# Optimization experiments

Hardware: AMD Instinct MI355X
Metric: run time of the kernel (lower is better)

The kernel has to match this reference:

```python
import jax, jax.numpy as jnp
import numpy as np

# --- architecture constants (match init_kwargs) ---
SLEN = 104
PTILE = 8
STEP = 2
N_BANDS = 2
MAX_DET = 2
N_SRC_PARAMS = 2
ENC_C = 20
ENC_HIDDEN = 256
# dim_out_all = 0.5*D*(D+1)*(4+2*n_source_params) + 1 + D  (probs over n_sources + per-count loc/flux mean+logvar)
DIM_OUT = int(0.5 * MAX_DET * (MAX_DET + 1) * (4 + 2 * N_SRC_PARAMS)) + 1 + MAX_DET  # 27


def _p(key, shape, scale=0.02):
    return scale * jax.random.normal(key, shape, dtype=jnp.float32)


def setup_inputs() -> dict:
    key = jax.random.key(0)
    ks = jax.random.split(key, 14)
    flat_in = ENC_C * PTILE * PTILE  # 20*8*8 = 1280
    return {
        "images": jax.random.normal(ks[0], (32, N_BANDS, SLEN, SLEN), dtype=jnp.float32),
        "conv1_w": _p(ks[1], (ENC_C, N_BANDS, 3, 3)),
        "conv1_b": _p(ks[2], (ENC_C,)),
        "conv2_w": _p(ks[3], (ENC_C, ENC_C, 3, 3)),
        "conv2_b": _p(ks[4], (ENC_C,)),
        "fc1_w": _p(ks[5], (ENC_HIDDEN, flat_in)),
        "fc1_b": _p(ks[6], (ENC_HIDDEN,)),
        "fc2_w": _p(ks[7], (ENC_HIDDEN, ENC_HIDDEN)),
        "fc2_b": _p(ks[8], (ENC_HIDDEN,)),
        "fc3_w": _p(ks[9], (ENC_HIDDEN, ENC_HIDDEN)),
        "fc3_b": _p(ks[10], (ENC_HIDDEN,)),
        "fcf_w": _p(ks[11], (DIM_OUT, ENC_HIDDEN)),
        "fcf_b": _p(ks[12], (DIM_OUT,)),
    }


def _tile_images(images):
    # torch tile_images: (B, C, slen, slen) -> (B * n_ptiles, C, P, P), tiles row-major over (x, y)
    B, C = images.shape[0], images.shape[1]
    patches = jax.lax.conv_general_dilated_patches(
        images, filter_shape=(PTILE, PTILE), window_strides=(STEP, STEP), padding="VALID"
    )  # (B, C*P*P, Hn, Wn) with feature dim ordered (C, P, P)
    Hn, Wn = patches.shape[2], patches.shape[3]
    p = patches.reshape(B, C, PTILE, PTILE, Hn, Wn)
    p = p.transpose(0, 4, 5, 1, 2, 3)  # (B, Hn, Wn, C, P, P)
    return p.reshape(B * Hn * Wn, C, PTILE, PTILE)


def _conv(x, w, b):
    y = jax.lax.conv_general_dilated(
        x, w, window_strides=(1, 1), padding="SAME",
        dimension_numbers=("NCHW", "OIHW", "NCHW"),
    )
    return y + b[None, :, None, None]


def reference(images, conv1_w, conv1_b, conv2_w, conv2_b,
              fc1_w, fc1_b, fc2_w, fc2_b, fc3_w, fc3_b, fcf_w, fcf_b):
    ptiles = _tile_images(images)                       # (B*nT, C, P, P)
    h = jax.nn.relu(_conv(ptiles, conv1_w, conv1_b))    # (B*nT, 20, P, P)
    h = jax.nn.relu(_conv(h, conv2_w, conv2_b))
    h = h.reshape(h.shape[0], -1)                       # Flatten -> (B*nT, 1280)
    h = jax.nn.relu(h @ fc1_w.T + fc1_b)
    h = jax.nn.relu(h @ fc2_w.T + fc2_b)
    h = jax.nn.relu(h @ fc3_w.T + fc3_b)
    return h @ fcf_w.T + fcf_b                          # (B*nT, dim_out_all)
```

## Files before the change

kernel.cpp:

```cpp
#include <hip/hip_runtime.h>
#include <hip/hip_bf16.h>

#define NPATCH 76832
#define NBLK   601
#define K1     1280

typedef __attribute__((ext_vector_type(8))) short  short8;
typedef __attribute__((ext_vector_type(4))) float  floatx4;

__device__ __forceinline__ unsigned short f2b(float f) {
    unsigned int u = __builtin_bit_cast(unsigned int, f);
    u += 0x7FFFu + ((u >> 16) & 1u);
    return (unsigned short)(u >> 16);
}
__device__ __forceinline__ unsigned int pk2(float a, float b) {
    __hip_bfloat162 h = __float22bfloat162_rn(make_float2(a, b));
    unsigned int u;
    __builtin_memcpy(&u, &h, 4);
    return u;
}

__device__ __forceinline__ void gload_lds16(const unsigned short* g, unsigned short* l) {
    __builtin_amdgcn_global_load_lds(
        (__attribute__((address_space(1))) void*)g,
        (__attribute__((address_space(3))) void*)l,
        16, 0, 0);
}

__device__ __host__ __forceinline__ int swz8(int row, int i) {
    return (((row & 1) * 4 + i) ^ ((row >> 1) & 7));
}

__global__ void prep_small(const float* __restrict__ c1w, const float* __restrict__ c2w,
                           unsigned short* __restrict__ W1T, unsigned short* __restrict__ W2T) {
    int i = blockIdx.x * 256 + threadIdx.x;
    if (i < 1024) {
        int o = i >> 5, k = i & 31;
        unsigned short v = 0;
        if (o < 20 && k < 18) v = f2b(c1w[o * 18 + k]);
        W1T[(o >> 1) * 64 + swz8(o, k >> 3) * 8 + (k & 7)] = v;
        return;
    }
    i -= 1024;
    if (i < 9216) {
        int tap = i >> 10, rem = i & 1023, o = rem >> 5, c = rem & 31;
        unsigned short v = 0;
        if (o < 20 && c < 20) v = f2b(c2w[o * 180 + c * 9 + tap]);
        W2T[tap * 1024 + (o >> 1) * 64 + swz8(o, c >> 3) * 8 + (c & 7)] = v;
    }
}

__global__ __launch_bounds__(256, 3) void conv_mfma(
    const float* __restrict__ img,
    const unsigned short* __restrict__ W1T, const float* __restrict__ b1,
    const unsigned short* __restrict__ W2T, const float* __restrict__ b2,
    unsigned short* __restrict__ X, int row0,
    const float* __restrict__ f1w, const float* __restrict__ f2w,
    const float* __restrict__ f3w, const float* __restrict__ ffw,
    unsigned short* __restrict__ W1F, unsigned short* __restrict__ W2F,
    unsigned short* __restrict__ W3F, unsigned short* __restrict__ WfF)
{
    __shared__ alignas(16) unsigned short s_buf[8 * 2048 + 64];
    __shared__ alignas(16) unsigned short s_w1t[1024];
    __shared__ alignas(16) unsigned short s_w2t[9216];
    __shared__ float s_b1[32], s_b2[32];
    constexpr int ZOFF = 8 * 2048;

    const int tid = threadIdx.x;
    for (int d = tid; d < 512; d += 256)  ((unsigned int*)s_w1t)[d] = ((const unsigned int*)W1T)[d];
    for (int d = tid; d < 4608; d += 256) ((unsigned int*)s_w2t)[d] = ((const unsigned int*)W2T)[d];
    if (tid < 32) {
        ((unsigned int*)&s_buf[ZOFF])[tid] = 0u;
        s_b1[tid] = (tid < 20) ? b1[tid] : 0.f;
        s_b2[tid] = (tid < 20) ? b2[tid] : 0.f;
    }

    const int q = tid >> 5, t = tid & 31;
    const int Pl = blockIdx.x * 8 + q;
    const int Pi = row0 + Pl;
    const bool valid = Pi < NPATCH;
    int b = 0, hi = 0, wi = 0;
    if (valid) { b = Pi / 2401; int rem = Pi - b * 2401; hi = rem / 49; wi = rem - hi * 49; }
    const int py = t >> 2, px0 = (t & 3) * 2;
    const float* ib = img + (long long)b * 21632 + (hi * 2) * 104 + (wi * 2);

    float win[2][3][4];
    #pragma unroll
    for (int c = 0; c < 2; ++c)
        #pragma unroll
        for (int dy = 0; dy < 3; ++dy) {
            int ny = py + dy - 1;
            int nyc = ny < 0 ? 0 : (ny > 7 ? 7 : ny);
            #pragma unroll
            for (int dxw = 0; dxw < 4; ++dxw) {
                int nx = px0 + dxw - 1;
                int nxc = nx < 0 ? 0 : (nx > 7 ? 7 : nx);
                win[c][dy][dxw] = ib[c * 10816 + nyc * 104 + nxc];
            }
        }

    #pragma unroll
    for (int j = 0; j < 2; ++j) {
        const int px = px0 + j, pl = py * 8 + px;
        float val[18];
        #pragma unroll
        for (int c = 0; c < 2; ++c)
            #pragma unroll
            for (int dy = 0; dy < 3; ++dy) {
                int ny = py + dy - 1;
                bool rok = valid && ((unsigned)ny < 8u);
                #pragma unroll
                for (int dx = 0; dx < 3; ++dx) {
                    int nx = px + dx - 1;
                    bool ok = rok && ((unsigned)nx < 8u);
                    val[c * 9 + dy * 3 + dx] = ok ? win[c][dy][dx + j] : 0.f;
                }
            }
        alignas(16) unsigned int au[16];
        #pragma unroll
        for (int i = 0; i < 9; ++i) au[i] = pk2(val[2 * i], val[2 * i + 1]);
        #pragma unroll
        for (int i = 9; i < 16; ++i) au[i] = 0u;
        unsigned short* base = &s_buf[q * 2048 + (pl >> 1) * 64];
        #pragma unroll
        for (int i = 0; i < 4; ++i)
            *(uint4*)&base[swz8(pl, i) * 8] = ((const uint4*)au)[i];
    }
    __syncthreads();

    const int wave = tid >> 6, lane = tid & 63;
    const int l15 = lane & 15, quad = lane >> 4;
    const int p0 = wave * 2;

    int boffB[2];
    #pragma unroll
    for (int i = 0; i < 2; ++i) {
        int oo = i * 16 + l15;
        boffB[i] = (oo >> 1) * 64 + swz8(oo, quad) * 8;
    }

    short8 a1f[2];
    #pragma unroll
    for (int mt = 0; mt < 2; ++mt) a1f[mt] = *(const short8*)&s_w1t[boffB[mt]];

    floatx4 acc1[2][2][4] = {};
    #pragma unroll
    for (int pp = 0; pp < 2; ++pp)
        #pragma unroll
        for (int nt = 0; nt < 4; ++nt) {
            int pix = nt * 16 + l15;
            short8 pf = *(const short8*)&s_buf[(p0 + pp) * 2048 + (pix >> 1) * 64 + swz8(pix, quad) * 8];
            #pragma unroll
            for (int mt = 0; mt < 2; ++mt)
                acc1[pp][mt][nt] = __builtin_amdgcn_mfma_f32_16x16x32_bf16(a1f[mt], pf, acc1[pp][mt][nt], 0, 0, 0);
        }

    float bv1[2][4];
    #pragma unroll
    for (int mt = 0; mt < 2; ++mt)
        #pragma unroll
        for (int r = 0; r < 4; ++r) bv1[mt][r] = s_b1[mt * 16 + quad * 4 + r];

    #pragma unroll
    for (int pp = 0; pp < 2; ++pp)
        #pragma unroll
        for (int mt = 0; mt < 2; ++mt)
            #pragma unroll
            for (int nt = 0; nt < 4; ++nt) {
                floatx4 v = acc1[pp][mt][nt];
                uint2 w;
                w.x = pk2(fmaxf(v[0] + bv1[mt][0], 0.f), fmaxf(v[1] + bv1[mt][1], 0.f));
                w.y = pk2(fmaxf(v[2] + bv1[mt][2], 0.f), fmaxf(v[3] + bv1[mt][3], 0.f));
                int pix = nt * 16 + l15;
                int off = (p0 + pp) * 2048 + (pix >> 1) * 64
                        + swz8(pix, mt * 2 + (quad >> 1)) * 8 + (quad & 1) * 4;
                *(uint2*)&s_buf[off] = w;
            }

    int syv[4], pxv[4];
    #pragma unroll
    for (int mt = 0; mt < 4; ++mt) { int p = mt * 16 + l15; syv[mt] = p >> 3; pxv[mt] = p & 7; }

    floatx4 acc2[2][4][2] = {};
    #pragma unroll 1
    for (int dy = 0; dy < 3; ++dy) {
        int sy[4]; bool okY[4];
        #pragma unroll
        for (int mt = 0; mt < 4; ++mt) {
            sy[mt] = syv[mt] + dy - 1;
            okY[mt] = (unsigned)sy[mt] < 8u;
        }
        #pragma unroll
        for (int dx = 0; dx < 3; ++dx) {
            const int tap = dy * 3 + dx;
            short8 bf0 = *(const short8*)&s_w2t[tap * 1024 + boffB[0]];
            short8 bf1 = *(const short8*)&s_w2t[tap * 1024 + boffB[1]];
            #pragma unroll
            for (int mt = 0; mt < 4; ++mt) {
                int sx = pxv[mt] + dx - 1;
                bool ok = okY[mt] & ((unsigned)sx < 8u);
                int ps = sy[mt] * 8 + sx;
                int offl = (ps >> 1) * 64 + swz8(ps, quad) * 8;
                #pragma unroll
                for (int pp = 0; pp < 2; ++pp) {
                    int off = ok ? ((p0 + pp) * 2048 + offl) : (ZOFF + quad * 8);
                    short8 af = *(const short8*)&s_buf[off];
                    acc2[pp][mt][0] = __builtin_amdgcn_mfma_f32_16x16x32_bf16(af, bf0, acc2[pp][mt][0], 0, 0, 0);
                    acc2[pp][mt][1] = __builtin_amdgcn_mfma_f32_16x16x32_bf16(af, bf1, acc2[pp][mt][1], 0, 0, 0);
                }
            }
        }
    }

    #pragma unroll
    for (int pp = 0; pp < 2; ++pp) {
        unsigned short* xrow = X + (long long)(blockIdx.x * 8 + p0 + pp) * K1;
        #pragma unroll
        for (int nt = 0; nt < 2; ++nt) {
            const int col = nt * 16 + l15;
            if (col < 20) {
                const float bv = s_b2[col];
                #pragma unroll
                for (int mt = 0; mt < 4; ++mt) {
                    floatx4 v = acc2[pp][mt][nt];
                    uint2 w;
                    w.x = pk2(fmaxf(v[0] + bv, 0.f), fmaxf(v[1] + bv, 0.f));
                    w.y = pk2(fmaxf(v[2] + bv, 0.f), fmaxf(v[3] + bv, 0.f));
                    *(uint2*)&xrow[col * 64 + mt * 16 + quad * 4] = w;
                }
            }
        }
    }

    if (row0 == 0 && blockIdx.x < 800) {
        const int bb_ = blockIdx.x;
        if (bb_ < 256) {
            const int o = bb_;
            const int obase = ((o >> 6) * 4 + ((o >> 4) & 3)) * 512 + (o & 15) * 8;
            #pragma unroll
            for (int j = 0; j < 5; ++j) {
                int k = tid + 256 * j;
                int dst = (k >> 5) * 8192 + obase + ((k >> 3) & 3) * 128 + (k & 7);
                W1F[dst] = f2b(f1w[o * 1280 + k]);
            }
        } else if (bb_ < 512) {
            const int o = bb_ - 256, k = tid;
            int dst = ((k >> 5) * 16 + (o >> 6) * 4 + ((o >> 4) & 3)) * 512
                    + (((k >> 3) & 3) * 16 + (o & 15)) * 8 + (k & 7);
            W2F[dst] = f2b(f2w[o * 256 + k]);
        } else if (bb_ < 768) {
            const int o = bb_ - 512, k = tid;
            int dst = ((k >> 5) * 16 + (o >> 6) * 4 + ((o >> 4) & 3)) * 512
                    + (((k >> 3) & 3) * 16 + (o & 15)) * 8 + (k & 7);
            W3F[dst] = f2b(f3w[o * 256 + k]);
        } else {
            const int o = bb_ - 768, k = tid;
            unsigned short v = (o < 27) ? f2b(ffw[o * 256 + k]) : (unsigned short)0;
            int dst = ((k >> 5) * 2 + (o >> 4)) * 512
                    + (((k >> 3) & 3) * 16 + (o & 15)) * 8 + (k & 7);
            WfF[dst] = v;
        }
    }
}

__global__ __launch_bounds__(256, 3) void fc_all(
    const unsigned short* __restrict__ X,
    const unsigned short* __restrict__ W1F, const unsigned short* __restrict__ W2F,
    const unsigned short* __restrict__ W3F, const unsigned short* __restrict__ WfF,
    const float* __restrict__ b1, const float* __restrict__ b2,
    const float* __restrict__ b3, const float* __restrict__ bf_,
    float* __restrict__ out, int row0)
{
    __shared__ alignas(16) unsigned short s_mem[16384];

    const int tid = threadIdx.x;
    const int m0 = blockIdx.x * 64;
    const int wave = tid >> 6, lane = tid & 63;
    const int l15 = lane & 15, quad = lane >> 4;

    floatx4 acc[4][4];
    #pragma unroll
    for (int mt = 0; mt < 4; ++mt)
        #pragma unroll
        for (int nt = 0; nt < 4; ++nt) acc[mt][nt] = floatx4{0.f, 0.f, 0.f, 0.f};

    const unsigned short* xsrc = X + (long long)(m0 + wave * 16 + l15) * 1280 + quad * 8;
    auto stage = [&](int buf, int c) {
        unsigned short* dst = &s_mem[buf * 4096 + wave * 512];
        gload_lds16(xsrc + (2 * c) * 32, dst);
        gload_lds16(xsrc + (2 * c + 1) * 32, dst + 2048);
    };

    stage(0, 0);
    __syncthreads();
    #pragma unroll 2
    for (int c = 0; c < 20; ++c) {
        short8 af[2][4];
        #pragma unroll
        for (int kh = 0; kh < 2; ++kh)
            #pragma unroll
            for (int mt = 0; mt < 4; ++mt)
                af[kh][mt] = *(const short8*)(W1F + (((2 * c + kh) * 16) + wave * 4 + mt) * 512 + lane * 8);
        __builtin_amdgcn_sched_barrier(0);
        if (c < 19) stage((c + 1) & 1, c + 1);
        const int bb = (c & 1) * 4096;
        __builtin_amdgcn_s_setprio(1);
        #pragma unroll
        for (int kh = 0; kh < 2; ++kh) {
            short8 bf[4];
            #pragma unroll
            for (int nt = 0; nt < 4; ++nt)
                bf[nt] = *(const short8*)&s_mem[bb + (kh * 4 + nt) * 512 + lane * 8];
            #pragma unroll
            for (int mt = 0; mt < 4; ++mt)
                #pragma unroll
                for (int nt = 0; nt < 4; ++nt)
                    acc[mt][nt] = __builtin_amdgcn_mfma_f32_16x16x32_bf16(af[kh][mt], bf[nt], acc[mt][nt], 0, 0, 0);
        }
        __builtin_amdgcn_s_setprio(0);
        __syncthreads();
    }

    #pragma unroll
    for (int mt = 0; mt < 4; ++mt) {
        const int obase = wave * 64 + mt * 16 + quad * 4;
        const float v0 = b1[obase], v1 = b1[obase + 1], v2 = b1[obase + 2], v3 = b1[obase + 3];
        const int slot = (wave * 2 + (mt >> 1)) * 4;
        const int qk = (mt & 1) * 2 + (quad >> 1);
        #pragma unroll
        for (int nt = 0; nt < 4; ++nt) {
            floatx4 v = acc[mt][nt];
            uint2 w;
            w.x = pk2(fmaxf(v[0] + v0, 0.f), fmaxf(v[1] + v1, 0.f));
            w.y = pk2(fmaxf(v[2] + v2, 0.f), fmaxf(v[3] + v3, 0.f));
            *(uint2*)&s_mem[(slot + nt) * 512 + qk * 128 + l15 * 8 + (quad & 1) * 4] = w;
        }
    }
    __syncthreads();

    #pragma unroll 1
    for (int layer = 0; layer < 2; ++layer) {
        const unsigned short* Wp = (layer == 0) ? W2F : W3F;
        const float* bp = (layer == 0) ? b2 : b3;

        #pragma unroll
        for (int mt = 0; mt < 4; ++mt)
            #pragma unroll
            for (int nt = 0; nt < 4; ++nt) acc[mt][nt] = floatx4{0.f, 0.f, 0.f, 0.f};

        short8 afc[4];
        #pragma unroll
        for (int mt = 0; mt < 4; ++mt)
            afc[mt] = *(const short8*)(Wp + (wave * 4 + mt) * 512 + lane * 8);

        #pragma unroll
        for (int it = 0; it < 8; ++it) {
            short8 afn[4];
            if (it < 7) {
                #pragma unroll
                for (int mt = 0; mt < 4; ++mt)
                    afn[mt] = *(const short8*)(Wp + ((it + 1) * 16 + wave * 4 + mt) * 512 + lane * 8);
            }
            short8 bf[4];
            #pragma unroll
            for (int nt = 0; nt < 4; ++nt)
                bf[nt] = *(const short8*)&s_mem[(it * 4 + nt) * 512 + lane * 8];
            __builtin_amdgcn_s_setprio(1);
            #pragma unroll
            for (int mt = 0; mt < 4; ++mt)
                #pragma unroll
                for (int nt = 0; nt < 4; ++nt)
                    acc[mt][nt] = __builtin_amdgcn_mfma_f32_16x16x32_bf16(afc[mt], bf[nt], acc[mt][nt], 0, 0, 0);
            __builtin_amdgcn_s_setprio(0);
            if (it < 7) {
                #pragma unroll
                for (int mt = 0; mt < 4; ++mt) afc[mt] = afn[mt];
            }
        }
        __syncthreads();
        #pragma unroll
        for (int mt = 0; mt < 4; ++mt) {
            const int obase = wave * 64 + mt * 16 + quad * 4;
            const float v0 = bp[obase], v1 = bp[obase + 1], v2 = bp[obase + 2], v3 = bp[obase + 3];
            const int slot = (wave * 2 + (mt >> 1)) * 4;
            const int qk = (mt & 1) * 2 + (quad >> 1);
            #pragma unroll
            for (int nt = 0; nt < 4; ++nt) {
                floatx4 v = acc[mt][nt];
                uint2 w;
                w.x = pk2(fmaxf(v[0] + v0, 0.f), fmaxf(v[1] + v1, 0.f));
                w.y = pk2(fmaxf(v[2] + v2, 0.f), fmaxf(v[3] + v3, 0.f));
                *(uint2*)&s_mem[(slot + nt) * 512 + qk * 128 + l15 * 8 + (quad & 1) * 4] = w;
            }
        }
        __syncthreads();
    }

    floatx4 accf[2] = {floatx4{0.f, 0.f, 0.f, 0.f}, floatx4{0.f, 0.f, 0.f, 0.f}};
    const int myrow = wave * 16 + l15;
    #pragma unroll
    for (int w8 = 0; w8 < 8; ++w8) {
        short8 bfr = *(const short8*)&s_mem[(w8 * 4 + wave) * 512 + lane * 8];
        #pragma unroll
        for (int mt = 0; mt < 2; ++mt) {
            short8 afr = *(const short8*)(WfF + (w8 * 2 + mt) * 512 + lane * 8);
            accf[mt] = __builtin_amdgcn_mfma_f32_16x16x32_bf16(afr, bfr, accf[mt], 0, 0, 0);
        }
    }
    const int grow = row0 + m0 + myrow;
    if (grow < NPATCH) {
        #pragma unroll
        for (int mt = 0; mt < 2; ++mt) {
            #pragma unroll
            for (int r = 0; r < 4; ++r) {
                int o = mt * 16 + quad * 4 + r;
                if (o < 27)
                    out[(long long)grow * 27 + o] = accf[mt][r] + bf_[o];
            }
        }
    }
}

extern "C" void kernel_launch(void* const* d_in, const int* in_sizes, int n_in,
                              void* d_out, int out_size, void* d_ws, size_t ws_size,
                              hipStream_t stream) {
    const float* images = (const float*)d_in[0];
    const float* c1w = (const float*)d_in[1];
    const float* c1b = (const float*)d_in[2];
    const float* c2w = (const float*)d_in[3];
    const float* c2b = (const float*)d_in[4];
    const float* f1w = (const float*)d_in[5];
    const float* f1b = (const float*)d_in[6];
    const float* f2w = (const float*)d_in[7];
    const float* f2b_ = (const float*)d_in[8];
    const float* f3w = (const float*)d_in[9];
    const float* f3b = (const float*)d_in[10];
    const float* ffw = (const float*)d_in[11];
    const float* ffb = (const float*)d_in[12];

    const long long W1_E = 327680, W2_E = 65536, W3_E = 65536;
    const long long W1T_E = 1024, W2T_E = 9216, WF_E = 8192;
    const long long WB = (W1_E + W2_E + W3_E + W1T_E + W2T_E + WF_E) * 2;
    char* ws = (char*)d_ws;
    unsigned short* W1F = (unsigned short*)ws;
    unsigned short* W2F = W1F + W1_E;
    unsigned short* W3F = W2F + W2_E;
    unsigned short* W1T = W3F + W3_E;
    unsigned short* W2T = W1T + W1T_E;
    unsigned short* WfF = W2T + W2T_E;
    unsigned short* X   = (unsigned short*)(ws + WB);

    long long avail = (long long)ws_size - WB - 256;
    int nb_max = (int)(avail / 327680LL);
    if (nb_max < 1) nb_max = 1;
    if (nb_max > NBLK) nb_max = NBLK;
    int nchunks = (NBLK + nb_max - 1) / nb_max;
    int nb_even = (NBLK + nchunks - 1) / nchunks;

    prep_small<<<40, 256, 0, stream>>>(c1w, c2w, W1T, W2T);

    for (int b0 = 0; b0 < NBLK; b0 += nb_even) {
        int nb = NBLK - b0; if (nb > nb_even) nb = nb_even;
        int row0 = b0 * 128;
        int rows = nb * 128;

        conv_mfma<<<rows / 8, 256, 0, stream>>>(images, W1T, c1b, W2T, c2b, X, row0,
                                                f1w, f2w, f3w, ffw, W1F, W2F, W3F, WfF);
        fc_all<<<rows / 64, 256, 0, stream>>>(X, W1F, W2F, W3F, WfF,
                                              f1b, f2b_, f3b, ffb, (float*)d_out, row0);
    }
}
```

Baseline: 294.2 us.

## Fuse conv and FC stages into one persistent cooperative kernel with grid sync

Replaces the prep, conv and FC kernel launches with a single persistent cooperative kernel. Each block first builds the conv weights into LDS once, then loops over conv work items while also converting the FC weights to bf16, and afterwards passes a grid-wide barrier before looping over FC tiles. This is meant to remove launch overhead, the separate prep kernel and the per-work-item weight staging, and to keep all CUs busy through persistent scheduling. In exchange, occupancy is capped by the cooperative grid size and the large LDS footprint, and the grid sync serializes the two phases. The old multi-kernel path stays as a fallback if the cooperative launch fails.

```diff
diff --git a/kernel.cpp b/kernel.cpp
--- a/kernel.cpp
+++ b/kernel.cpp
@@ -1,9 +1,14 @@
 #include <hip/hip_runtime.h>
 #include <hip/hip_bf16.h>
+#include <hip/hip_cooperative_groups.h>
+
+namespace cg = cooperative_groups;
 
 #define NPATCH 76832
 #define NBLK   601
 #define K1     1280
+#define NCONVW (NBLK * 16)
+#define NFCW   ((NBLK * 128) / 64)
 
 typedef __attribute__((ext_vector_type(8))) short  short8;
 typedef __attribute__((ext_vector_type(4))) float  floatx4;
@@ -19,16 +24,393 @@
     __builtin_memcpy(&u, &h, 4);
     return u;
 }
-
 __device__ __forceinline__ void gload_lds16(const unsigned short* g, unsigned short* l) {
     __builtin_amdgcn_global_load_lds(
         (__attribute__((address_space(1))) void*)g,
         (__attribute__((address_space(3))) void*)l,
         16, 0, 0);
 }
-
 __device__ __host__ __forceinline__ int swz8(int row, int i) {
     return (((row & 1) * 4 + i) ^ ((row >> 1) & 7));
+}
+
+__global__ __launch_bounds__(256, 3) void fused(
+    const float* __restrict__ img,
+    const float* __restrict__ c1w, const float* __restrict__ c1b,
+    const float* __restrict__ c2w, const float* __restrict__ c2b,
+    const float* __restrict__ f1w, const float* __restrict__ f2w,
+    const float* __restrict__ f3w, const float* __restrict__ ffw,
+    const float* __restrict__ f1b, const float* __restrict__ f2b_,
+    const float* __restrict__ f3b, const float* __restrict__ ffb,
+    unsigned short* __restrict__ W1F, unsigned short* __restrict__ W2F,
+    unsigned short* __restrict__ W3F, unsigned short* __restrict__ WfF,
+    unsigned short* __restrict__ X, float* __restrict__ out)
+{
+    __shared__ alignas(16) unsigned short s_lds[26816];
+    unsigned short* s_buf = s_lds;
+    unsigned short* s_w1t = s_lds + 16448;
+    unsigned short* s_w2t = s_lds + 17472;
+    float* s_b1 = (float*)(s_lds + 26688);
+    float* s_b2 = (float*)(s_lds + 26752);
+    constexpr int ZOFF = 8 * 2048;
+
+    const int tid = threadIdx.x;
+
+    for (int i = tid; i < 1024; i += 256) {
+        int o = i >> 5, k = i & 31;
+        bool ok = (o < 20) && (k < 18);
+        float raw = c1w[ok ? o * 18 + k : 0];
+        s_w1t[(o >> 1) * 64 + swz8(o, k >> 3) * 8 + (k & 7)] = ok ? f2b(raw) : (unsigned short)0;
+    }
+    for (int i = tid; i < 9216; i += 256) {
+        int tap = i >> 10, rem = i & 1023, o = rem >> 5, c = rem & 31;
+        bool ok = (o < 20) && (c < 20);
+        float raw = c2w[ok ? o * 180 + c * 9 + tap : 0];
+        s_w2t[tap * 1024 + (o >> 1) * 64 + swz8(o, c >> 3) * 8 + (c & 7)] = ok ? f2b(raw) : (unsigned short)0;
+    }
+    if (tid < 32) {
+        ((unsigned int*)&s_buf[ZOFF])[tid] = 0u;
+        s_b1[tid] = (tid < 20) ? c1b[tid] : 0.f;
+        s_b2[tid] = (tid < 20) ? c2b[tid] : 0.f;
+    }
+    __syncthreads();
+
+    const int q = tid >> 5, t = tid & 31;
+    const int wave = tid >> 6, lane = tid & 63;
+    const int l15 = lane & 15, quad = lane >> 4;
+    const int p0 = wave * 2;
+    const int py = t >> 2, px0 = (t & 3) * 2;
+
+    int boffB[2];
+    #pragma unroll
+    for (int i = 0; i < 2; ++i) {
+        int oo = i * 16 + l15;
+        boffB[i] = (oo >> 1) * 64 + swz8(oo, quad) * 8;
+    }
+    short8 a1f[2];
+    #pragma unroll
+    for (int mt = 0; mt < 2; ++mt) a1f[mt] = *(const short8*)&s_w1t[boffB[mt]];
+    float bv1[2][4];
+    #pragma unroll
+    for (int mt = 0; mt < 2; ++mt)
+        #pragma unroll
+        for (int r = 0; r < 4; ++r) bv1[mt][r] = s_b1[mt * 16 + quad * 4 + r];
+    int syv[4], pxv[4];
+    #pragma unroll
+    for (int mt = 0; mt < 4; ++mt) { int p = mt * 16 + l15; syv[mt] = p >> 3; pxv[mt] = p & 7; }
+
+    #pragma unroll 1
+    for (int wi = blockIdx.x; wi < NCONVW; wi += gridDim.x) {
+        const int Pi = wi * 8 + q;
+        const bool valid = Pi < NPATCH;
+        int b = 0, hi = 0, iwx = 0;
+        if (valid) { b = Pi / 2401; int rem = Pi - b * 2401; hi = rem / 49; iwx = rem - hi * 49; }
+        const float* ib = img + (long long)b * 21632 + (hi * 2) * 104 + (iwx * 2);
+
+        float win[2][3][4];
+        #pragma unroll
+        for (int c = 0; c < 2; ++c)
+            #pragma unroll
+            for (int dy = 0; dy < 3; ++dy) {
+                int ny = py + dy - 1;
+                int nyc = ny < 0 ? 0 : (ny > 7 ? 7 : ny);
+                #pragma unroll
+                for (int dxw = 0; dxw < 4; ++dxw) {
+                    int nx = px0 + dxw - 1;
+                    int nxc = nx < 0 ? 0 : (nx > 7 ? 7 : nx);
+                    win[c][dy][dxw] = ib[c * 10816 + nyc * 104 + nxc];
+                }
+            }
+
+        #pragma unroll
+        for (int j = 0; j < 2; ++j) {
+            const int px = px0 + j, pl = py * 8 + px;
+            float val[18];
+            #pragma unroll
+            for (int c = 0; c < 2; ++c)
+                #pragma unroll
+                for (int dy = 0; dy < 3; ++dy) {
+                    int ny = py + dy - 1;
+                    bool rok = valid && ((unsigned)ny < 8u);
+                    #pragma unroll
+                    for (int dx = 0; dx < 3; ++dx) {
+                        int nx = px + dx - 1;
+                        bool ok = rok && ((unsigned)nx < 8u);
+                        val[c * 9 + dy * 3 + dx] = ok ? win[c][dy][dx + j] : 0.f;
+                    }
+                }
+            alignas(16) unsigned int au[16];
+            #pragma unroll
+            for (int i = 0; i < 9; ++i) au[i] = pk2(val[2 * i], val[2 * i + 1]);
+            #pragma unroll
+            for (int i = 9; i < 16; ++i) au[i] = 0u;
+            unsigned short* base = &s_buf[q * 2048 + (pl >> 1) * 64];
+            #pragma unroll
+            for (int i = 0; i < 4; ++i)
+                *(uint4*)&base[swz8(pl, i) * 8] = ((const uint4*)au)[i];
+        }
+
+        floatx4 acc1[2][2][4] = {};
+        #pragma unroll
+        for (int pp = 0; pp < 2; ++pp)
+            #pragma unroll
+            for (int nt = 0; nt < 4; ++nt) {
+                int pix = nt * 16 + l15;
+                short8 pf = *(const short8*)&s_buf[(p0 + pp) * 2048 + (pix >> 1) * 64 + swz8(pix, quad) * 8];
+                #pragma unroll
+                for (int mt = 0; mt < 2; ++mt)
+                    acc1[pp][mt][nt] = __builtin_amdgcn_mfma_f32_16x16x32_bf16(a1f[mt], pf, acc1[pp][mt][nt], 0, 0, 0);
+            }
+
+        #pragma unroll
+        for (int pp = 0; pp < 2; ++pp)
+            #pragma unroll
+            for (int mt = 0; mt < 2; ++mt)
+                #pragma unroll
+                for (int nt = 0; nt < 4; ++nt) {
+                    floatx4 v = acc1[pp][mt][nt];
+                    uint2 w;
+                    w.x = pk2(fmaxf(v[0] + bv1[mt][0], 0.f), fmaxf(v[1] + bv1[mt][1], 0.f));
+                    w.y = pk2(fmaxf(v[2] + bv1[mt][2], 0.f), fmaxf(v[3] + bv1[mt][3], 0.f));
+                    int pix = nt * 16 + l15;
+                    int off = (p0 + pp) * 2048 + (pix >> 1) * 64
+                            + swz8(pix, mt * 2 + (quad >> 1)) * 8 + (quad & 1) * 4;
+                    *(uint2*)&s_buf[off] = w;
+                }
+
+        floatx4 acc2[2][4][2] = {};
+        #pragma unroll 1
+        for (int dy = 0; dy < 3; ++dy) {
+            int sy[4]; bool okY[4];
+            #pragma unroll
+            for (int mt = 0; mt < 4; ++mt) {
+                sy[mt] = syv[mt] + dy - 1;
+                okY[mt] = (unsigned)sy[mt] < 8u;
+            }
+            #pragma unroll
+            for (int dx = 0; dx < 3; ++dx) {
+                const int tap = dy * 3 + dx;
+                short8 bf0 = *(const short8*)&s_w2t[tap * 1024 + boffB[0]];
+                short8 bf1 = *(const short8*)&s_w2t[tap * 1024 + boffB[1]];
+                #pragma unroll
+                for (int mt = 0; mt < 4; ++mt) {
+                    int sx = pxv[mt] + dx - 1;
+                    bool ok = okY[mt] & ((unsigned)sx < 8u);
+                    int ps = sy[mt] * 8 + sx;
+                    int offl = (ps >> 1) * 64 + swz8(ps, quad) * 8;
+                    #pragma unroll
+                    for (int pp = 0; pp < 2; ++pp) {
+                        int off = ok ? ((p0 + pp) * 2048 + offl) : (ZOFF + quad * 8);
+                        short8 af = *(const short8*)&s_buf[off];
+                        acc2[pp][mt][0] = __builtin_amdgcn_mfma_f32_16x16x32_bf16(af, bf0, acc2[pp][mt][0], 0, 0, 0);
+                        acc2[pp][mt][1] = __builtin_amdgcn_mfma_f32_16x16x32_bf16(af, bf1, acc2[pp][mt][1], 0, 0, 0);
+                    }
+                }
+            }
+        }
+
+        #pragma unroll
+        for (int pp = 0; pp < 2; ++pp) {
+            unsigned short* xrow = X + (long long)(wi * 8 + p0 + pp) * K1;
+            #pragma unroll
+            for (int nt = 0; nt < 2; ++nt) {
+                const int col = nt * 16 + l15;
+                if (col < 20) {
+                    const float bv = s_b2[col];
+                    #pragma unroll
+                    for (int mt = 0; mt < 4; ++mt) {
+                        floatx4 v = acc2[pp][mt][nt];
+                        uint2 w;
+                        w.x = pk2(fmaxf(v[0] + bv, 0.f), fmaxf(v[1] + bv, 0.f));
+                        w.y = pk2(fmaxf(v[2] + bv, 0.f), fmaxf(v[3] + bv, 0.f));
+                        *(uint2*)&xrow[col * 64 + mt * 16 + quad * 4] = w;
+                    }
+                }
+            }
+        }
+
+        if (wi < 800) {
+            const int bb_ = wi;
+            if (bb_ < 256) {
+                const int o = bb_;
+                const int obase = ((o >> 6) * 4 + ((o >> 4) & 3)) * 512 + (o & 15) * 8;
+                #pragma unroll
+                for (int j = 0; j < 5; ++j) {
+                    int k = tid + 256 * j;
+                    int dst = (k >> 5) * 8192 + obase + ((k >> 3) & 3) * 128 + (k & 7);
+                    W1F[dst] = f2b(f1w[o * 1280 + k]);
+                }
+            } else if (bb_ < 512) {
+                const int o = bb_ - 256, k = tid;
+                int dst = ((k >> 5) * 16 + (o >> 6) * 4 + ((o >> 4) & 3)) * 512
+                        + (((k >> 3) & 3) * 16 + (o & 15)) * 8 + (k & 7);
+                W2F[dst] = f2b(f2w[o * 256 + k]);
+            } else if (bb_ < 768) {
+                const int o = bb_ - 512, k = tid;
+                int dst = ((k >> 5) * 16 + (o >> 6) * 4 + ((o >> 4) & 3)) * 512
+                        + (((k >> 3) & 3) * 16 + (o & 15)) * 8 + (k & 7);
+                W3F[dst] = f2b(f3w[o * 256 + k]);
+            } else {
+                const int o = bb_ - 768, k = tid;
+                unsigned short v = (o < 27) ? f2b(ffw[o * 256 + k]) : (unsigned short)0;
+                int dst = ((k >> 5) * 2 + (o >> 4)) * 512
+                        + (((k >> 3) & 3) * 16 + (o & 15)) * 8 + (k & 7);
+                WfF[dst] = v;
+            }
+        }
+    }
+
+    __threadfence();
+    cg::this_grid().sync();
+
+    unsigned short* s_mem = s_lds;
+    #pragma unroll 1
+    for (int wj = blockIdx.x; wj < NFCW; wj += gridDim.x) {
+        const int m0 = wj * 64;
+
+        floatx4 acc[4][4];
+        #pragma unroll
+        for (int mt = 0; mt < 4; ++mt)
+            #pragma unroll
+            for (int nt = 0; nt < 4; ++nt) acc[mt][nt] = floatx4{0.f, 0.f, 0.f, 0.f};
+
+        const unsigned short* xsrc = X + (long long)(m0 + wave * 16 + l15) * 1280 + quad * 8;
+        auto stage = [&](int buf, int c) {
+            unsigned short* dst = &s_mem[buf * 4096 + wave * 512];
+            gload_lds16(xsrc + (2 * c) * 32, dst);
+            gload_lds16(xsrc + (2 * c + 1) * 32, dst + 2048);
+        };
+
+        stage(0, 0);
+        __syncthreads();
+        #pragma unroll 2
+        for (int c = 0; c < 20; ++c) {
+            short8 af[2][4];
+            #pragma unroll
+            for (int kh = 0; kh < 2; ++kh)
+                #pragma unroll
+                for (int mt = 0; mt < 4; ++mt)
+                    af[kh][mt] = *(const short8*)(W1F + (((2 * c + kh) * 16) + wave * 4 + mt) * 512 + lane * 8);
+            __builtin_amdgcn_sched_barrier(0);
+            if (c < 19) stage((c + 1) & 1, c + 1);
+            const int bb = (c & 1) * 4096;
+            __builtin_amdgcn_s_setprio(1);
+            #pragma unroll
+            for (int kh = 0; kh < 2; ++kh) {
+                short8 bf[4];
+                #pragma unroll
+                for (int nt = 0; nt < 4; ++nt)
+                    bf[nt] = *(const short8*)&s_mem[bb + (kh * 4 + nt) * 512 + lane * 8];
+                #pragma unroll
+                for (int mt = 0; mt < 4; ++mt)
+                    #pragma unroll
+                    for (int nt = 0; nt < 4; ++nt)
+                        acc[mt][nt] = __builtin_amdgcn_mfma_f32_16x16x32_bf16(af[kh][mt], bf[nt], acc[mt][nt], 0, 0, 0);
+            }
+            __builtin_amdgcn_s_setprio(0);
+            __syncthreads();
+        }
+
+        #pragma unroll
+        for (int mt = 0; mt < 4; ++mt) {
+            const int obase = wave * 64 + mt * 16 + quad * 4;
+            const float v0 = f1b[obase], v1 = f1b[obase + 1], v2 = f1b[obase + 2], v3 = f1b[obase + 3];
+            const int slot = (wave * 2 + (mt >> 1)) * 4;
+            const int qk = (mt & 1) * 2 + (quad >> 1);
+            #pragma unroll
+            for (int nt = 0; nt < 4; ++nt) {
+                floatx4 v = acc[mt][nt];
+                uint2 w;
+                w.x = pk2(fmaxf(v[0] + v0, 0.f), fmaxf(v[1] + v1, 0.f));
+                w.y = pk2(fmaxf(v[2] + v2, 0.f), fmaxf(v[3] + v3, 0.f));
+                *(uint2*)&s_mem[(slot + nt) * 512 + qk * 128 + l15 * 8 + (quad & 1) * 4] = w;
+            }
+        }
+        __syncthreads();
+
+        #pragma unroll 1
+        for (int layer = 0; layer < 2; ++layer) {
+            const unsigned short* Wp = (layer == 0) ? W2F : W3F;
+            const float* bp = (layer == 0) ? f2b_ : f3b;
+
+            #pragma unroll
+            for (int mt = 0; mt < 4; ++mt)
+                #pragma unroll
+                for (int nt = 0; nt < 4; ++nt) acc[mt][nt] = floatx4{0.f, 0.f, 0.f, 0.f};
+
+            short8 afc[4];
+            #pragma unroll
+            for (int mt = 0; mt < 4; ++mt)
+                afc[mt] = *(const short8*)(Wp + (wave * 4 + mt) * 512 + lane * 8);
+
+            #pragma unroll
+            for (int it = 0; it < 8; ++it) {
+                short8 afn[4];
+                if (it < 7) {
+                    #pragma unroll
+                    for (int mt = 0; mt < 4; ++mt)
+                        afn[mt] = *(const short8*)(Wp + ((it + 1) * 16 + wave * 4 + mt) * 512 + lane * 8);
+                }
+                short8 bf[4];
+                #pragma unroll
+                for (int nt = 0; nt < 4; ++nt)
+                    bf[nt] = *(const short8*)&s_mem[(it * 4 + nt) * 512 + lane * 8];
+                __builtin_amdgcn_s_setprio(1);
+                #pragma unroll
+                for (int mt = 0; mt < 4; ++mt)
+                    #pragma unroll
+                    for (int nt = 0; nt < 4; ++nt)
+                        acc[mt][nt] = __builtin_amdgcn_mfma_f32_16x16x32_bf16(afc[mt], bf[nt], acc[mt][nt], 0, 0, 0);
+                __builtin_amdgcn_s_setprio(0);
+                if (it < 7) {
+                    #pragma unroll
+                    for (int mt = 0; mt < 4; ++mt) afc[mt] = afn[mt];
+                }
+            }
+            __syncthreads();
+            #pragma unroll
+            for (int mt = 0; mt < 4; ++mt) {
+                const int obase = wave * 64 + mt * 16 + quad * 4;
+                const float v0 = bp[obase], v1 = bp[obase + 1], v2 = bp[obase + 2], v3 = bp[obase + 3];
+                const int slot = (wave * 2 + (mt >> 1)) * 4;
+                const int qk = (mt & 1) * 2 + (quad >> 1);
+                #pragma unroll
+                for (int nt = 0; nt < 4; ++nt) {
+                    floatx4 v = acc[mt][nt];
+                    uint2 w;
+                    w.x = pk2(fmaxf(v[0] + v0, 0.f), fmaxf(v[1] + v1, 0.f));
+                    w.y = pk2(fmaxf(v[2] + v2, 0.f), fmaxf(v[3] + v3, 0.f));
+                    *(uint2*)&s_mem[(slot + nt) * 512 + qk * 128 + l15 * 8 + (quad & 1) * 4] = w;
+                }
+            }
+            __syncthreads();
+        }
+
+        floatx4 accf[2] = {floatx4{0.f, 0.f, 0.f, 0.f}, floatx4{0.f, 0.f, 0.f, 0.f}};
+        const int myrow = wave * 16 + l15;
+        #pragma unroll
+        for (int w8 = 0; w8 < 8; ++w8) {
+            short8 bfr = *(const short8*)&s_mem[(w8 * 4 + wave) * 512 + lane * 8];
+            #pragma unroll
+            for (int mt = 0; mt < 2; ++mt) {
+                short8 afr = *(const short8*)(WfF + (w8 * 2 + mt) * 512 + lane * 8);
+                accf[mt] = __builtin_amdgcn_mfma_f32_16x16x32_bf16(afr, bfr, accf[mt], 0, 0, 0);
+            }
+        }
+        const int grow = m0 + myrow;
+        if (grow < NPATCH) {
+            #pragma unroll
+            for (int mt = 0; mt < 2; ++mt) {
+                #pragma unroll
+                for (int r = 0; r < 4; ++r) {
+                    int o = mt * 16 + quad * 4 + r;
+                    if (o < 27)
+                        out[(long long)grow * 27 + o] = accf[mt][r] + ffb[o];
+                }
+            }
+        }
+        __syncthreads();
+    }
 }
 
 __global__ void prep_small(const float* __restrict__ c1w, const float* __restrict__ c2w,
@@ -449,24 +831,29 @@
     unsigned short* W2T = W1T + W1T_E;
     unsigned short* WfF = W2T + W2T_E;
     unsigned short* X   = (unsigned short*)(ws + WB);
-
-    long long avail = (long long)ws_size - WB - 256;
-    int nb_max = (int)(avail / 327680LL);
-    if (nb_max < 1) nb_max = 1;
-    if (nb_max > NBLK) nb_max = NBLK;
-    int nchunks = (NBLK + nb_max - 1) / nb_max;
-    int nb_even = (NBLK + nchunks - 1) / nchunks;
+    float* outp = (float*)d_out;
+
+    int bpc = 0;
+    hipError_t qe = hipOccupancyMaxActiveBlocksPerMultiprocessor(&bpc, fused, 256, 0);
+    if (qe != hipSuccess || bpc < 1) bpc = 1;
+    if (bpc > 3) bpc = 3;
+    int grid = 256 * bpc;
+
+    void* kargs[] = {
+        (void*)&images, (void*)&c1w, (void*)&c1b, (void*)&c2w, (void*)&c2b,
+        (void*)&f1w, (void*)&f2w, (void*)&f3w, (void*)&ffw,
+        (void*)&f1b, (void*)&f2b_, (void*)&f3b, (void*)&ffb,
+        (void*)&W1F, (void*)&W2F, (void*)&W3F, (void*)&WfF,
+        (void*)&X, (void*)&outp
+    };
+    hipError_t e = hipLaunchCooperativeKernel((const void*)fused, dim3(grid), dim3(256),
+                                              kargs, 0, stream);
+    if (e == hipSuccess) return;
+    (void)hipGetLastError();
 
     prep_small<<<40, 256, 0, stream>>>(c1w, c2w, W1T, W2T);
-
-    for (int b0 = 0; b0 < NBLK; b0 += nb_even) {
-        int nb = NBLK - b0; if (nb > nb_even) nb = nb_even;
-        int row0 = b0 * 128;
-        int rows = nb * 128;
-
-        conv_mfma<<<rows / 8, 256, 0, stream>>>(images, W1T, c1b, W2T, c2b, X, row0,
-                                                f1w, f2w, f3w, ffw, W1F, W2F, W3F, WfF);
-        fc_all<<<rows / 64, 256, 0, stream>>>(X, W1F, W2F, W3F, WfF,
-                                              f1b, f2b_, f3b, ffb, (float*)d_out, row0);
-    }
+    conv_mfma<<<NBLK * 16, 256, 0, stream>>>(images, W1T, c1b, W2T, c2b, X, 0,
+                                             f1w, f2w, f3w, ffw, W1F, W2F, W3F, WfF);
+    fc_all<<<NFCW, 256, 0, stream>>>(X, W1F, W2F, W3F, WfF,
+                                     f1b, f2b_, f3b, ffb, outp, 0);
 }
```

New measurement: 665.3 us. 2.26x slower.
